# Performance work log

Measured on AMD Instinct MI355X. Metric: run time of the kernel, lower is better.

The kernel has to match this reference:

```python
import jax, jax.numpy as jnp
import numpy as np

VOCAB, EMB, HID = 32000, 128, 128
B, S = 8, 1024


def setup_inputs() -> dict:
    key = jax.random.key(0)
    ks = jax.random.split(key, 8)
    scale_e = 1.0  # nn.Embedding default N(0,1)
    k_rnn = 1.0 / np.sqrt(HID)  # nn.RNN uniform(-1/sqrt(H), 1/sqrt(H))
    k_fc = 1.0 / np.sqrt(HID)
    return {
        "x": jax.random.randint(ks[0], (B, S), 0, VOCAB),
        "emb_table": jax.random.normal(ks[1], (VOCAB, EMB), dtype=jnp.float32) * scale_e,
        "W_ih": jax.random.uniform(ks[2], (HID, EMB), jnp.float32, -k_rnn, k_rnn),
        "b_ih": jax.random.uniform(ks[3], (HID,), jnp.float32, -k_rnn, k_rnn),
        "W_hh": jax.random.uniform(ks[4], (HID, HID), jnp.float32, -k_rnn, k_rnn),
        "b_hh": jax.random.uniform(ks[5], (HID,), jnp.float32, -k_rnn, k_rnn),
        "fc_W": jax.random.uniform(ks[6], (VOCAB, HID), jnp.float32, -k_fc, k_fc),
        "fc_b": jax.random.uniform(ks[7], (VOCAB,), jnp.float32, -k_fc, k_fc),
    }


def reference(x, emb_table, W_ih, b_ih, W_hh, b_hh, fc_W, fc_b):
    # Embedding lookup: [B,S,E]
    e = emb_table[x]
    # Precompute input projection for all timesteps: [B,S,H]
    x_proj = jnp.einsum("bse,he->bsh", e, W_ih) + b_ih + b_hh

    h0 = jnp.zeros((x.shape[0], W_hh.shape[0]), dtype=e.dtype)

    def step(h, xp_t):  # xp_t: [B,H]
        h_new = jnp.tanh(xp_t + h @ W_hh.T)
        return h_new, h_new

    # scan over time: xs [S,B,H]
    h_last, hs = jax.lax.scan(step, h0, jnp.swapaxes(x_proj, 0, 1))
    outputs = jnp.swapaxes(hs, 0, 1)  # [B,S,H]
    logits = jnp.einsum("bsh,vh->bsv", outputs, fc_W) + fc_b  # [B,S,V]
    hidden_state = h_last[None]  # [1,B,H] matching torch num_layers dim
    return logits, hidden_state
```

## Files before the change

kernel.cpp:

```cpp
#include <hip/hip_runtime.h>
#include <hip/hip_bf16.h>

#define VOCAB 32000
#define EMB   128
#define HID   128
#define BB    8
#define SS    1024

typedef __bf16 bf16x8_t __attribute__((ext_vector_type(8)));
typedef float  f32x4_t  __attribute__((ext_vector_type(4)));

__device__ __forceinline__ float dpp_xor1(float x) {
    return __int_as_float(__builtin_amdgcn_update_dpp(
        0, __float_as_int(x), 0xB1, 0xF, 0xF, true));
}
__device__ __forceinline__ float dpp_xor2(float x) {
    return __int_as_float(__builtin_amdgcn_update_dpp(
        0, __float_as_int(x), 0x4E, 0xF, 0xF, true));
}

__global__ __launch_bounds__(512) void xproj_kernel(
    const int* __restrict__ x, const float* __restrict__ emb,
    const float* __restrict__ W_ih, const float* __restrict__ b_ih,
    const float* __restrict__ b_hh, float* __restrict__ xp)
{
    const int t  = threadIdx.x;
    const int h  = t >> 2;
    const int ks = t & 3;

    float w[32];
    {
        const float* wr = W_ih + h * EMB + ks * 32;
        #pragma unroll
        for (int i = 0; i < 32; i += 4) {
            float4 v = *(const float4*)(wr + i);
            w[i] = v.x; w[i+1] = v.y; w[i+2] = v.z; w[i+3] = v.w;
        }
    }
    const float bias = b_ih[h] + b_hh[h];

    __shared__ float el[2][EMB];
    const int base = blockIdx.x * 32;

    float4 v = make_float4(0.f, 0.f, 0.f, 0.f);
    if (t < 32) v = *(const float4*)(emb + (size_t)x[base] * EMB + t * 4);

    for (int r = 0; r < 32; ++r) {
        if (t < 32) *(float4*)(&el[r & 1][t * 4]) = v;
        __syncthreads();
        if (t < 32 && r + 1 < 32)
            v = *(const float4*)(emb + (size_t)x[base + r + 1] * EMB + t * 4);

        float a0 = 0.f, a1 = 0.f, a2 = 0.f, a3 = 0.f;
        const float* e = &el[r & 1][ks * 32];
        #pragma unroll
        for (int c = 0; c < 8; ++c) {
            float4 hv = *(const float4*)(e + c * 4);
            a0 = fmaf(w[c*4+0], hv.x, a0);
            a1 = fmaf(w[c*4+1], hv.y, a1);
            a2 = fmaf(w[c*4+2], hv.z, a2);
            a3 = fmaf(w[c*4+3], hv.w, a3);
        }
        float sum = (a0 + a1) + (a2 + a3);
        sum += __shfl_xor(sum, 1);
        sum += __shfl_xor(sum, 2);
        if (ks == 0) xp[(size_t)(base + r) * HID + h] = bias + sum;
    }
}

__global__ __launch_bounds__(256) void convert_bf16_kernel(
    const float* __restrict__ in, __hip_bfloat16* __restrict__ out)
{
    const size_t i = ((size_t)blockIdx.x * 256 + threadIdx.x) * 8;
    float4 a = *(const float4*)(in + i);
    float4 b = *(const float4*)(in + i + 4);
    union { __hip_bfloat16 h[8]; uint4 u; } p;
    p.h[0] = __float2bfloat16(a.x); p.h[1] = __float2bfloat16(a.y);
    p.h[2] = __float2bfloat16(a.z); p.h[3] = __float2bfloat16(a.w);
    p.h[4] = __float2bfloat16(b.x); p.h[5] = __float2bfloat16(b.y);
    p.h[6] = __float2bfloat16(b.z); p.h[7] = __float2bfloat16(b.w);
    *(uint4*)(out + i) = p.u;
}

__global__ __launch_bounds__(256) void rnn_kernel(
    const float* __restrict__ xp, const float* __restrict__ W_hh,
    __hip_bfloat16* __restrict__ hs_bf16, float* __restrict__ hidden_out)
{
    const int b  = blockIdx.x;
    const int t  = threadIdx.x;
    const int w  = t >> 6;
    const int l  = t & 63;
    const int ks = l & 3;
    const int g  = l >> 2;
    const int jb = w * 16 + g;

    f32x4_t wr[2][8];
    #pragma unroll
    for (int m = 0; m < 2; ++m) {
        const float* src = W_hh + (size_t)(jb + 64 * m) * HID + ks * 32;
        #pragma unroll
        for (int i = 0; i < 8; ++i) wr[m][i] = *(const f32x4_t*)(src + i * 4);
    }

    __shared__ float hbuf[2][160];
    if (t < 160) hbuf[0][t] = 0.f;

    const float* xpb = xp + (size_t)b * SS * HID;
    const bool  wrt  = (ks == 0);

    float xsA[8][2], xsB[8][2];
    if (wrt) {
        #pragma unroll
        for (int u = 0; u < 8; ++u) {
            xsA[u][0] = xpb[(size_t)u * HID + jb];
            xsA[u][1] = xpb[(size_t)u * HID + jb + 64];
        }
    }
    __syncthreads();

    const int rbase = ks * 40;

#define RNN_SUPERSTEP(XC, XN, BASE)                                          \
    {                                                                        \
        const int nbase_ = (BASE) + 8;                                       \
        if (wrt && nbase_ < SS) {                                            \
            _Pragma("unroll")                                                \
            for (int u = 0; u < 8; ++u) {                                    \
                XN[u][0] = xpb[(size_t)(nbase_ + u) * HID + jb];             \
                XN[u][1] = xpb[(size_t)(nbase_ + u) * HID + jb + 64];        \
            }                                                                \
        }                                                                    \
        _Pragma("unroll")                                                    \
        for (int u = 0; u < 8; ++u) {                                        \
            const int step_ = (BASE) + u;                                    \
            const float* hc_ = hbuf[u & 1];                                  \
            f32x4_t hv[8];                                                   \
            _Pragma("unroll")                                                \
            for (int i = 0; i < 4; ++i)                                      \
                hv[i] = *(const f32x4_t*)(hc_ + rbase + i * 4);              \
            _Pragma("unroll")                                                \
            for (int i = 4; i < 8; ++i)                                      \
                hv[i] = *(const f32x4_t*)(hc_ + rbase + 4 + i * 4);          \
            f32x4_t a0 = {0.f,0.f,0.f,0.f}, a1 = a0, c0 = a0, c1 = a0;       \
            _Pragma("unroll")                                                \
            for (int i = 0; i < 4; ++i) {                                    \
                a0 += wr[0][i]   * hv[i];                                    \
                a1 += wr[0][i+4] * hv[i+4];                                  \
                c0 += wr[1][i]   * hv[i];                                    \
                c1 += wr[1][i+4] * hv[i+4];                                  \
            }                                                                \
            f32x4_t av = a0 + a1, cv = c0 + c1;                              \
            float s0 = (av.x + av.y) + (av.z + av.w);                        \
            float s1 = (cv.x + cv.y) + (cv.z + cv.w);                        \
            s0 += dpp_xor1(s0);  s0 += dpp_xor2(s0);                         \
            s1 += dpp_xor1(s1);  s1 += dpp_xor2(s1);                         \
            if (wrt) {                                                       \
                const float z0 = XC[u][0] + s0;                              \
                const float e0 = __expf(2.0f * z0);                          \
                const float h0 = 1.0f - 2.0f * __builtin_amdgcn_rcpf(e0 + 1.0f); \
                const float z1 = XC[u][1] + s1;                              \
                const float e1 = __expf(2.0f * z1);                          \
                const float h1 = 1.0f - 2.0f * __builtin_amdgcn_rcpf(e1 + 1.0f); \
                const int j0 = jb, j1 = jb + 64;                             \
                hbuf[(u + 1) & 1][j0 + ((j0 >> 4) << 2)] = h0;               \
                hbuf[(u + 1) & 1][j1 + ((j1 >> 4) << 2)] = h1;               \
                hs_bf16[((size_t)b * SS + step_) * HID + j0] = __float2bfloat16(h0); \
                hs_bf16[((size_t)b * SS + step_) * HID + j1] = __float2bfloat16(h1); \
                if (step_ == SS - 1) {                                       \
                    hidden_out[b * HID + j0] = h0;                           \
                    hidden_out[b * HID + j1] = h1;                           \
                }                                                            \
            }                                                                \
            asm volatile("s_waitcnt lgkmcnt(0)" ::: "memory");               \
            __builtin_amdgcn_s_barrier();                                    \
        }                                                                    \
    }

    for (int sb2 = 0; sb2 < SS / 16; ++sb2) {
        const int base = sb2 * 16;
        RNN_SUPERSTEP(xsA, xsB, base);
        RNN_SUPERSTEP(xsB, xsA, base + 8);
    }
#undef RNN_SUPERSTEP
}

__global__ __launch_bounds__(256) void fc_kernel(
    const __hip_bfloat16* __restrict__ A, const __hip_bfloat16* __restrict__ Wb,
    const float* __restrict__ fc_b, float* __restrict__ C)
{
    const int lane = threadIdx.x & 63;
    const int wv   = threadIdx.x >> 6;
    const int wm   = wv >> 1;
    const int wn   = wv & 1;

    const int bid = blockIdx.x;
    const int wg  = (bid & 7) * 2000 + (bid >> 3);
    const int mb  = wg / 250;
    const int nb  = wg % 250;

    const int m0 = mb * 128 + wm * 64;
    const int n0 = nb * 128 + wn * 64;
    const int lr = lane & 15;
    const int kq = lane >> 4;

    const __hip_bfloat16* Arow = A  + (size_t)(m0 + lr) * HID + kq * 8;
    const __hip_bfloat16* Wrow = Wb + (size_t)(n0 + lr) * HID + kq * 8;

    f32x4_t acc[4][4];
    #pragma unroll
    for (int i = 0; i < 4; ++i)
        #pragma unroll
        for (int jj = 0; jj < 4; ++jj)
            acc[i][jj] = (f32x4_t){0.f, 0.f, 0.f, 0.f};

    bf16x8_t af[2][4], bw[2][4];
    #pragma unroll
    for (int mt = 0; mt < 4; ++mt) af[0][mt] = *(const bf16x8_t*)(Arow + mt * 16 * HID);
    #pragma unroll
    for (int nt = 0; nt < 4; ++nt) bw[0][nt] = *(const bf16x8_t*)(Wrow + nt * 16 * HID);

    #pragma unroll
    for (int kk = 0; kk < 4; ++kk) {
        const int cur = kk & 1, nxt = cur ^ 1;
        if (kk < 3) {
            const int off = (kk + 1) * 32;
            #pragma unroll
            for (int mt = 0; mt < 4; ++mt)
                af[nxt][mt] = *(const bf16x8_t*)(Arow + mt * 16 * HID + off);
            #pragma unroll
            for (int nt = 0; nt < 4; ++nt)
                bw[nxt][nt] = *(const bf16x8_t*)(Wrow + nt * 16 * HID + off);
        }
        #pragma unroll
        for (int mt = 0; mt < 4; ++mt)
            #pragma unroll
            for (int nt = 0; nt < 4; ++nt)
                acc[mt][nt] = __builtin_amdgcn_mfma_f32_16x16x32_bf16(
                    bw[cur][nt], af[cur][mt], acc[mt][nt], 0, 0, 0);
    }

    const int vq = kq * 4;
    #pragma unroll
    for (int nt = 0; nt < 4; ++nt) {
        const int v0 = n0 + nt * 16 + vq;
        float4 fb = *(const float4*)(fc_b + v0);
        const f32x4_t fbv = {fb.x, fb.y, fb.z, fb.w};
        #pragma unroll
        for (int mt = 0; mt < 4; ++mt) {
            const int row = m0 + mt * 16 + lr;
            *(f32x4_t*)(C + (size_t)row * VOCAB + v0) = acc[mt][nt] + fbv;
        }
    }
}

extern "C" void kernel_launch(void* const* d_in, const int* in_sizes, int n_in,
                              void* d_out, int out_size, void* d_ws, size_t ws_size,
                              hipStream_t stream)
{
    const int*   x    = (const int*)  d_in[0];
    const float* emb  = (const float*)d_in[1];
    const float* W_ih = (const float*)d_in[2];
    const float* b_ih = (const float*)d_in[3];
    const float* W_hh = (const float*)d_in[4];
    const float* b_hh = (const float*)d_in[5];
    const float* fc_W = (const float*)d_in[6];
    const float* fc_b = (const float*)d_in[7];

    float* logits = (float*)d_out;
    float* hidden = logits + (size_t)BB * SS * VOCAB;

    char* ws = (char*)d_ws;
    float*           xpb = (float*)ws;
    __hip_bfloat16*  hsb = (__hip_bfloat16*)(ws + 4194304);
    __hip_bfloat16*  fwb = (__hip_bfloat16*)(ws + 6291456);

    xproj_kernel<<<dim3(256), dim3(512), 0, stream>>>(x, emb, W_ih, b_ih, b_hh, xpb);
    convert_bf16_kernel<<<dim3(2000), dim3(256), 0, stream>>>(fc_W, fwb);
    rnn_kernel<<<dim3(8), dim3(256), 0, stream>>>(xpb, W_hh, hsb, hidden);
    fc_kernel<<<dim3(16000), dim3(256), 0, stream>>>(hsb, fwb, fc_b, logits);
}
```

Measured before the change: 652.6 us.

## Rework RNN recurrence work split to four rows per lane group with 8-way K split

Each lane group now computes four consecutive hidden units and splits the 128-wide dot product across 8 lanes instead of 4, so each lane reads only 16 h values per step and reuses them across four weight rows. A third DPP reduction stage combines the 8 partial sums. Hidden-state stores to LDS and the bf16 output become vectorised 4-wide writes, and xproj prefetch becomes float4 loads. The goal is to shorten the serial per-step latency of the recurrence. In exchange, only 1 of 8 lanes does the tanh and stores, and the extra reduction stage adds latency.

New measurement: 718.7 us. 1.1x slower.

```diff
diff --git a/kernel.cpp b/kernel.cpp
--- a/kernel.cpp
+++ b/kernel.cpp
@@ -17,6 +17,10 @@
 __device__ __forceinline__ float dpp_xor2(float x) {
     return __int_as_float(__builtin_amdgcn_update_dpp(
         0, __float_as_int(x), 0x4E, 0xF, 0xF, true));
+}
+__device__ __forceinline__ float dpp_mir8(float x) {
+    return __int_as_float(__builtin_amdgcn_update_dpp(
+        0, __float_as_int(x), 0x141, 0xF, 0xF, true));
 }
 
 __global__ __launch_bounds__(512) void xproj_kernel(
@@ -82,7 +86,7 @@
     *(uint4*)(out + i) = p.u;
 }
 
-__global__ __launch_bounds__(256) void rnn_kernel(
+__global__ __launch_bounds__(256, 1) void rnn_kernel(
     const float* __restrict__ xp, const float* __restrict__ W_hh,
     __hip_bfloat16* __restrict__ hs_bf16, float* __restrict__ hidden_out)
 {
@@ -90,98 +94,105 @@
     const int t  = threadIdx.x;
     const int w  = t >> 6;
     const int l  = t & 63;
-    const int ks = l & 3;
-    const int g  = l >> 2;
-    const int jb = w * 16 + g;
-
-    f32x4_t wr[2][8];
-    #pragma unroll
-    for (int m = 0; m < 2; ++m) {
-        const float* src = W_hh + (size_t)(jb + 64 * m) * HID + ks * 32;
-        #pragma unroll
-        for (int i = 0; i < 8; ++i) wr[m][i] = *(const f32x4_t*)(src + i * 4);
-    }
+    const int ks = l & 7;
+    const int jg = l >> 3;
+    const int j0 = w * 32 + jg * 4;
+
+    f32x4_t wv[4][4];
+    #pragma unroll
+    for (int m = 0; m < 4; ++m) {
+        const float* src = W_hh + (size_t)(j0 + m) * HID + ks * 16;
+        #pragma unroll
+        for (int i = 0; i < 4; ++i) wv[m][i] = *(const f32x4_t*)(src + i * 4);
+    }
+    asm volatile("" :
+        "+v"(wv[0][0]), "+v"(wv[0][1]), "+v"(wv[0][2]), "+v"(wv[0][3]),
+        "+v"(wv[1][0]), "+v"(wv[1][1]), "+v"(wv[1][2]), "+v"(wv[1][3]),
+        "+v"(wv[2][0]), "+v"(wv[2][1]), "+v"(wv[2][2]), "+v"(wv[2][3]),
+        "+v"(wv[3][0]), "+v"(wv[3][1]), "+v"(wv[3][2]), "+v"(wv[3][3]));
 
     __shared__ float hbuf[2][160];
     if (t < 160) hbuf[0][t] = 0.f;
 
     const float* xpb = xp + (size_t)b * SS * HID;
     const bool  wrt  = (ks == 0);
-
-    float xsA[8][2], xsB[8][2];
+    const int   rb   = ks * 20;
+    const int   wb   = j0 + ((j0 >> 4) << 2);
+
+    float4 xsA[4], xsB[4];
     if (wrt) {
         #pragma unroll
-        for (int u = 0; u < 8; ++u) {
-            xsA[u][0] = xpb[(size_t)u * HID + jb];
-            xsA[u][1] = xpb[(size_t)u * HID + jb + 64];
-        }
+        for (int u = 0; u < 4; ++u)
+            xsA[u] = *(const float4*)(xpb + (size_t)u * HID + j0);
     }
     __syncthreads();
 
-    const int rbase = ks * 40;
-
-#define RNN_SUPERSTEP(XC, XN, BASE)                                          \
+#define RNN_SUPER4(XC, XN, BASE)                                             \
     {                                                                        \
-        const int nbase_ = (BASE) + 8;                                       \
-        if (wrt && nbase_ < SS) {                                            \
+        const int nb_ = (BASE) + 4;                                          \
+        if (wrt && nb_ < SS) {                                               \
             _Pragma("unroll")                                                \
-            for (int u = 0; u < 8; ++u) {                                    \
-                XN[u][0] = xpb[(size_t)(nbase_ + u) * HID + jb];             \
-                XN[u][1] = xpb[(size_t)(nbase_ + u) * HID + jb + 64];        \
-            }                                                                \
+            for (int u = 0; u < 4; ++u)                                      \
+                XN[u] = *(const float4*)(xpb + (size_t)(nb_ + u) * HID + j0);\
         }                                                                    \
         _Pragma("unroll")                                                    \
-        for (int u = 0; u < 8; ++u) {                                        \
+        for (int u = 0; u < 4; ++u) {                                        \
             const int step_ = (BASE) + u;                                    \
             const float* hc_ = hbuf[u & 1];                                  \
-            f32x4_t hv[8];                                                   \
-            _Pragma("unroll")                                                \
-            for (int i = 0; i < 4; ++i)                                      \
-                hv[i] = *(const f32x4_t*)(hc_ + rbase + i * 4);              \
-            _Pragma("unroll")                                                \
-            for (int i = 4; i < 8; ++i)                                      \
-                hv[i] = *(const f32x4_t*)(hc_ + rbase + 4 + i * 4);          \
-            f32x4_t a0 = {0.f,0.f,0.f,0.f}, a1 = a0, c0 = a0, c1 = a0;       \
-            _Pragma("unroll")                                                \
-            for (int i = 0; i < 4; ++i) {                                    \
-                a0 += wr[0][i]   * hv[i];                                    \
-                a1 += wr[0][i+4] * hv[i+4];                                  \
-                c0 += wr[1][i]   * hv[i];                                    \
-                c1 += wr[1][i+4] * hv[i+4];                                  \
-            }                                                                \
-            f32x4_t av = a0 + a1, cv = c0 + c1;                              \
-            float s0 = (av.x + av.y) + (av.z + av.w);                        \
-            float s1 = (cv.x + cv.y) + (cv.z + cv.w);                        \
-            s0 += dpp_xor1(s0);  s0 += dpp_xor2(s0);                         \
-            s1 += dpp_xor1(s1);  s1 += dpp_xor2(s1);                         \
+            f32x4_t hv0 = *(const f32x4_t*)(hc_ + rb);                       \
+            f32x4_t hv1 = *(const f32x4_t*)(hc_ + rb + 4);                   \
+            f32x4_t hv2 = *(const f32x4_t*)(hc_ + rb + 8);                   \
+            f32x4_t hv3 = *(const f32x4_t*)(hc_ + rb + 12);                  \
+            f32x4_t a0 = wv[0][0] * hv0;                                     \
+            f32x4_t a1 = wv[1][0] * hv0;                                     \
+            f32x4_t a2 = wv[2][0] * hv0;                                     \
+            f32x4_t a3 = wv[3][0] * hv0;                                     \
+            a0 += wv[0][1] * hv1;  a1 += wv[1][1] * hv1;                     \
+            a2 += wv[2][1] * hv1;  a3 += wv[3][1] * hv1;                     \
+            a0 += wv[0][2] * hv2;  a1 += wv[1][2] * hv2;                     \
+            a2 += wv[2][2] * hv2;  a3 += wv[3][2] * hv2;                     \
+            a0 += wv[0][3] * hv3;  a1 += wv[1][3] * hv3;                     \
+            a2 += wv[2][3] * hv3;  a3 += wv[3][3] * hv3;                     \
+            float s0 = (a0.x + a0.y) + (a0.z + a0.w);                        \
+            float s1 = (a1.x + a1.y) + (a1.z + a1.w);                        \
+            float s2 = (a2.x + a2.y) + (a2.z + a2.w);                        \
+            float s3 = (a3.x + a3.y) + (a3.z + a3.w);                        \
+            s0 += dpp_xor1(s0); s1 += dpp_xor1(s1);                          \
+            s2 += dpp_xor1(s2); s3 += dpp_xor1(s3);                          \
+            s0 += dpp_xor2(s0); s1 += dpp_xor2(s1);                          \
+            s2 += dpp_xor2(s2); s3 += dpp_xor2(s3);                          \
+            s0 += dpp_mir8(s0); s1 += dpp_mir8(s1);                          \
+            s2 += dpp_mir8(s2); s3 += dpp_mir8(s3);                          \
             if (wrt) {                                                       \
-                const float z0 = XC[u][0] + s0;                              \
-                const float e0 = __expf(2.0f * z0);                          \
+                const float4 xc = XC[u];                                     \
+                const float z0 = xc.x + s0, z1 = xc.y + s1;                  \
+                const float z2 = xc.z + s2, z3 = xc.w + s3;                  \
+                const float e0 = __expf(2.0f * z0), e1 = __expf(2.0f * z1);  \
+                const float e2 = __expf(2.0f * z2), e3 = __expf(2.0f * z3);  \
                 const float h0 = 1.0f - 2.0f * __builtin_amdgcn_rcpf(e0 + 1.0f); \
-                const float z1 = XC[u][1] + s1;                              \
-                const float e1 = __expf(2.0f * z1);                          \
                 const float h1 = 1.0f - 2.0f * __builtin_amdgcn_rcpf(e1 + 1.0f); \
-                const int j0 = jb, j1 = jb + 64;                             \
-                hbuf[(u + 1) & 1][j0 + ((j0 >> 4) << 2)] = h0;               \
-                hbuf[(u + 1) & 1][j1 + ((j1 >> 4) << 2)] = h1;               \
-                hs_bf16[((size_t)b * SS + step_) * HID + j0] = __float2bfloat16(h0); \
-                hs_bf16[((size_t)b * SS + step_) * HID + j1] = __float2bfloat16(h1); \
-                if (step_ == SS - 1) {                                       \
-                    hidden_out[b * HID + j0] = h0;                           \
-                    hidden_out[b * HID + j1] = h1;                           \
-                }                                                            \
+                const float h2 = 1.0f - 2.0f * __builtin_amdgcn_rcpf(e2 + 1.0f); \
+                const float h3 = 1.0f - 2.0f * __builtin_amdgcn_rcpf(e3 + 1.0f); \
+                *(f32x4_t*)(&hbuf[(u + 1) & 1][wb]) = (f32x4_t){h0, h1, h2, h3}; \
+                union { __hip_bfloat16 q[4]; uint2 u2; } pk;                 \
+                pk.q[0] = __float2bfloat16(h0); pk.q[1] = __float2bfloat16(h1); \
+                pk.q[2] = __float2bfloat16(h2); pk.q[3] = __float2bfloat16(h3); \
+                *(uint2*)(&hs_bf16[((size_t)b * SS + step_) * HID + j0]) = pk.u2; \
+                if (step_ == SS - 1)                                         \
+                    *(float4*)(&hidden_out[b * HID + j0]) =                  \
+                        make_float4(h0, h1, h2, h3);                         \
             }                                                                \
             asm volatile("s_waitcnt lgkmcnt(0)" ::: "memory");               \
             __builtin_amdgcn_s_barrier();                                    \
         }                                                                    \
     }
 
-    for (int sb2 = 0; sb2 < SS / 16; ++sb2) {
-        const int base = sb2 * 16;
-        RNN_SUPERSTEP(xsA, xsB, base);
-        RNN_SUPERSTEP(xsB, xsA, base + 8);
-    }
-#undef RNN_SUPERSTEP
+    for (int sb = 0; sb < SS / 8; ++sb) {
+        const int base = sb * 8;
+        RNN_SUPER4(xsA, xsB, base);
+        RNN_SUPER4(xsB, xsA, base + 4);
+    }
+#undef RNN_SUPER4
 }
 
 __global__ __launch_bounds__(256) void fc_kernel(
```

## Fuse RNN recurrence and FC GEMM into persistent kernel with progress flags

Applied to the files above, without the earlier changes.

Merges the sequential RNN kernel and the output projection GEMM into one persistent launch. Eight blocks run the recurrence and publish per-batch progress every 128 timesteps through atomic flags. The remaining 248 blocks spin-wait on those flags and compute logits for each finished chunk, so the large FC GEMM overlaps the latency-bound recurrence. The risks are deadlock if the RNN blocks are not co-resident, spin-wait overhead, and the GEMM traffic slowing the RNN critical path.

Result: faster. 556.7 us (-14.7%).

```diff
diff --git a/kernel.cpp b/kernel.cpp
--- a/kernel.cpp
+++ b/kernel.cpp
@@ -82,43 +82,47 @@
     *(uint4*)(out + i) = p.u;
 }
 
-__global__ __launch_bounds__(256) void rnn_kernel(
+__global__ __launch_bounds__(256) void mega_kernel(
     const float* __restrict__ xp, const float* __restrict__ W_hh,
-    __hip_bfloat16* __restrict__ hs_bf16, float* __restrict__ hidden_out)
+    __hip_bfloat16* __restrict__ hs_bf16, float* __restrict__ hidden_out,
+    const __hip_bfloat16* __restrict__ Wb, const float* __restrict__ fc_b,
+    float* __restrict__ C, unsigned int* __restrict__ prog)
 {
-    const int b  = blockIdx.x;
-    const int t  = threadIdx.x;
-    const int w  = t >> 6;
-    const int l  = t & 63;
-    const int ks = l & 3;
-    const int g  = l >> 2;
-    const int jb = w * 16 + g;
-
-    f32x4_t wr[2][8];
-    #pragma unroll
-    for (int m = 0; m < 2; ++m) {
-        const float* src = W_hh + (size_t)(jb + 64 * m) * HID + ks * 32;
+    const int bid = blockIdx.x;
+
+    if (bid < BB) {
+        const int b  = bid;
+        const int t  = threadIdx.x;
+        const int w  = t >> 6;
+        const int l  = t & 63;
+        const int ks = l & 3;
+        const int g  = l >> 2;
+        const int jb = w * 16 + g;
+
+        f32x4_t wr[2][8];
         #pragma unroll
-        for (int i = 0; i < 8; ++i) wr[m][i] = *(const f32x4_t*)(src + i * 4);
-    }
-
-    __shared__ float hbuf[2][160];
-    if (t < 160) hbuf[0][t] = 0.f;
-
-    const float* xpb = xp + (size_t)b * SS * HID;
-    const bool  wrt  = (ks == 0);
-
-    float xsA[8][2], xsB[8][2];
-    if (wrt) {
-        #pragma unroll
-        for (int u = 0; u < 8; ++u) {
-            xsA[u][0] = xpb[(size_t)u * HID + jb];
-            xsA[u][1] = xpb[(size_t)u * HID + jb + 64];
-        }
-    }
-    __syncthreads();
-
-    const int rbase = ks * 40;
+        for (int m = 0; m < 2; ++m) {
+            const float* src = W_hh + (size_t)(jb + 64 * m) * HID + ks * 32;
+            #pragma unroll
+            for (int i = 0; i < 8; ++i) wr[m][i] = *(const f32x4_t*)(src + i * 4);
+        }
+
+        __shared__ float hbuf[2][160];
+        if (t < 160) hbuf[0][t] = 0.f;
+
+        const float* xpb = xp + (size_t)b * SS * HID;
+        const bool  wrt  = (ks == 0);
+        const int rbase = ks * 40;
+
+        float xsA[8][2], xsB[8][2];
+        if (wrt) {
+            #pragma unroll
+            for (int u = 0; u < 8; ++u) {
+                xsA[u][0] = xpb[(size_t)u * HID + jb];
+                xsA[u][1] = xpb[(size_t)u * HID + jb + 64];
+            }
+        }
+        __syncthreads();
 
 #define RNN_SUPERSTEP(XC, XN, BASE)                                          \
     {                                                                        \
@@ -176,79 +180,100 @@
         }                                                                    \
     }
 
-    for (int sb2 = 0; sb2 < SS / 16; ++sb2) {
-        const int base = sb2 * 16;
-        RNN_SUPERSTEP(xsA, xsB, base);
-        RNN_SUPERSTEP(xsB, xsA, base + 8);
-    }
+        for (int chunk = 0; chunk < 8; ++chunk) {
+            for (int sb2 = 0; sb2 < 8; ++sb2) {
+                const int base = chunk * 128 + sb2 * 16;
+                RNN_SUPERSTEP(xsA, xsB, base);
+                RNN_SUPERSTEP(xsB, xsA, base + 8);
+            }
+            asm volatile("s_waitcnt vmcnt(0)" ::: "memory");
+            __builtin_amdgcn_s_barrier();
+            if (t == 0)
+                __hip_atomic_store(&prog[b], (unsigned)(chunk + 1),
+                                   __ATOMIC_RELEASE, __HIP_MEMORY_SCOPE_AGENT);
+        }
 #undef RNN_SUPERSTEP
-}
-
-__global__ __launch_bounds__(256) void fc_kernel(
-    const __hip_bfloat16* __restrict__ A, const __hip_bfloat16* __restrict__ Wb,
-    const float* __restrict__ fc_b, float* __restrict__ C)
-{
-    const int lane = threadIdx.x & 63;
-    const int wv   = threadIdx.x >> 6;
-    const int wm   = wv >> 1;
-    const int wn   = wv & 1;
-
-    const int bid = blockIdx.x;
-    const int wg  = (bid & 7) * 2000 + (bid >> 3);
-    const int mb  = wg / 250;
-    const int nb  = wg % 250;
-
-    const int m0 = mb * 128 + wm * 64;
-    const int n0 = nb * 128 + wn * 64;
-    const int lr = lane & 15;
-    const int kq = lane >> 4;
-
-    const __hip_bfloat16* Arow = A  + (size_t)(m0 + lr) * HID + kq * 8;
-    const __hip_bfloat16* Wrow = Wb + (size_t)(n0 + lr) * HID + kq * 8;
-
-    f32x4_t acc[4][4];
-    #pragma unroll
-    for (int i = 0; i < 4; ++i)
-        #pragma unroll
-        for (int jj = 0; jj < 4; ++jj)
-            acc[i][jj] = (f32x4_t){0.f, 0.f, 0.f, 0.f};
-
-    bf16x8_t af[2][4], bw[2][4];
-    #pragma unroll
-    for (int mt = 0; mt < 4; ++mt) af[0][mt] = *(const bf16x8_t*)(Arow + mt * 16 * HID);
-    #pragma unroll
-    for (int nt = 0; nt < 4; ++nt) bw[0][nt] = *(const bf16x8_t*)(Wrow + nt * 16 * HID);
-
-    #pragma unroll
-    for (int kk = 0; kk < 4; ++kk) {
-        const int cur = kk & 1, nxt = cur ^ 1;
-        if (kk < 3) {
-            const int off = (kk + 1) * 32;
-            #pragma unroll
-            for (int mt = 0; mt < 4; ++mt)
-                af[nxt][mt] = *(const bf16x8_t*)(Arow + mt * 16 * HID + off);
-            #pragma unroll
-            for (int nt = 0; nt < 4; ++nt)
-                bw[nxt][nt] = *(const bf16x8_t*)(Wrow + nt * 16 * HID + off);
-        }
-        #pragma unroll
-        for (int mt = 0; mt < 4; ++mt)
-            #pragma unroll
-            for (int nt = 0; nt < 4; ++nt)
-                acc[mt][nt] = __builtin_amdgcn_mfma_f32_16x16x32_bf16(
-                    bw[cur][nt], af[cur][mt], acc[mt][nt], 0, 0, 0);
-    }
-
-    const int vq = kq * 4;
-    #pragma unroll
-    for (int nt = 0; nt < 4; ++nt) {
-        const int v0 = n0 + nt * 16 + vq;
-        float4 fb = *(const float4*)(fc_b + v0);
-        const f32x4_t fbv = {fb.x, fb.y, fb.z, fb.w};
-        #pragma unroll
-        for (int mt = 0; mt < 4; ++mt) {
-            const int row = m0 + mt * 16 + lr;
-            *(f32x4_t*)(C + (size_t)row * VOCAB + v0) = acc[mt][nt] + fbv;
+    } else {
+        const int cid  = bid - BB;
+        const int NC   = 256 - BB;
+        const int t    = threadIdx.x;
+        const int lane = t & 63;
+        const int cw   = t >> 6;
+        const int wm   = cw >> 1;
+        const int wn   = cw & 1;
+        const int lr   = lane & 15;
+        const int kq   = lane >> 4;
+
+        for (int tc = 0; tc < 8; ++tc) {
+            if (t == 0) {
+                for (int b2 = 0; b2 < BB; ++b2) {
+                    while (__hip_atomic_fetch_add(&prog[b2], 0u,
+                               __ATOMIC_RELAXED, __HIP_MEMORY_SCOPE_AGENT)
+                           < (unsigned)(tc + 1))
+                        __builtin_amdgcn_s_sleep(32);
+                }
+            }
+            __syncthreads();
+            __builtin_amdgcn_fence(__ATOMIC_ACQUIRE, "agent");
+
+            for (int i = cid; i < 2000; i += NC) {
+                const int b2 = i / 250;
+                const int nb = i % 250;
+                const int mb = b2 * 8 + tc;
+                const int m0 = mb * 128 + wm * 64;
+                const int n0 = nb * 128 + wn * 64;
+
+                const __hip_bfloat16* Arow = hs_bf16 + (size_t)(m0 + lr) * HID + kq * 8;
+                const __hip_bfloat16* Wrow = Wb      + (size_t)(n0 + lr) * HID + kq * 8;
+
+                f32x4_t acc[4][4];
+                #pragma unroll
+                for (int ii = 0; ii < 4; ++ii)
+                    #pragma unroll
+                    for (int jj = 0; jj < 4; ++jj)
+                        acc[ii][jj] = (f32x4_t){0.f, 0.f, 0.f, 0.f};
+
+                bf16x8_t af[2][4], bw[2][4];
+                #pragma unroll
+                for (int mt = 0; mt < 4; ++mt)
+                    af[0][mt] = *(const bf16x8_t*)(Arow + mt * 16 * HID);
+                #pragma unroll
+                for (int nt = 0; nt < 4; ++nt)
+                    bw[0][nt] = *(const bf16x8_t*)(Wrow + nt * 16 * HID);
+
+                #pragma unroll
+                for (int kk = 0; kk < 4; ++kk) {
+                    const int cur = kk & 1, nxt = cur ^ 1;
+                    if (kk < 3) {
+                        const int off = (kk + 1) * 32;
+                        #pragma unroll
+                        for (int mt = 0; mt < 4; ++mt)
+                            af[nxt][mt] = *(const bf16x8_t*)(Arow + mt * 16 * HID + off);
+                        #pragma unroll
+                        for (int nt = 0; nt < 4; ++nt)
+                            bw[nxt][nt] = *(const bf16x8_t*)(Wrow + nt * 16 * HID + off);
+                    }
+                    #pragma unroll
+                    for (int mt = 0; mt < 4; ++mt)
+                        #pragma unroll
+                        for (int nt = 0; nt < 4; ++nt)
+                            acc[mt][nt] = __builtin_amdgcn_mfma_f32_16x16x32_bf16(
+                                bw[cur][nt], af[cur][mt], acc[mt][nt], 0, 0, 0);
+                }
+
+                const int vq = kq * 4;
+                #pragma unroll
+                for (int nt = 0; nt < 4; ++nt) {
+                    const int v0 = n0 + nt * 16 + vq;
+                    float4 fb = *(const float4*)(fc_b + v0);
+                    const f32x4_t fbv = {fb.x, fb.y, fb.z, fb.w};
+                    #pragma unroll
+                    for (int mt = 0; mt < 4; ++mt) {
+                        const int row = m0 + mt * 16 + lr;
+                        *(f32x4_t*)(C + (size_t)row * VOCAB + v0) = acc[mt][nt] + fbv;
+                    }
+                }
+            }
         }
     }
 }
@@ -273,9 +298,11 @@
     float*           xpb = (float*)ws;
     __hip_bfloat16*  hsb = (__hip_bfloat16*)(ws + 4194304);
     __hip_bfloat16*  fwb = (__hip_bfloat16*)(ws + 6291456);
-
+    unsigned int*    prg = (unsigned int*)(ws + 14483456);
+
+    hipMemsetAsync(prg, 0, 64, stream);
     xproj_kernel<<<dim3(256), dim3(512), 0, stream>>>(x, emb, W_ih, b_ih, b_hh, xpb);
     convert_bf16_kernel<<<dim3(2000), dim3(256), 0, stream>>>(fc_W, fwb);
-    rnn_kernel<<<dim3(8), dim3(256), 0, stream>>>(xpb, W_hh, hsb, hidden);
-    fc_kernel<<<dim3(16000), dim3(256), 0, stream>>>(hsb, fwb, fc_b, logits);
-}
+    mega_kernel<<<dim3(256), dim3(256), 0, stream>>>(xpb, W_hh, hsb, hidden,
+                                                     fwb, fc_b, logits, prg);
+}
```
